# Performance work log

Measured on AMD Instinct MI355X. Metric: run time of the kernel, lower is better.

## Reference

```python
import jax, jax.numpy as jnp
import numpy as np
import math

D = 256          # cubic grid size
THICKNESS = 20   # sponge thickness
DT = 0.001
N_PML = 2
R_PML = 0.001


def _build_sigma(vmax, shape, thickness):
    # vectorized equivalent of the torch slab-assignment loop:
    # final value at a point is damping(min distance to any face) if < thickness else 0
    sigma0 = -(N_PML + 1) * vmax * math.log(R_PML) / (2.0 * thickness)
    dists = []
    for ax, n in enumerate(shape):
        idx = jnp.arange(n)
        d = jnp.minimum(idx, n - 1 - idx)
        sh = [1, 1, 1]
        sh[ax] = n
        dists.append(d.reshape(sh))
    mind = jnp.minimum(jnp.minimum(
        jnp.broadcast_to(dists[0], shape),
        jnp.broadcast_to(dists[1], shape)),
        jnp.broadcast_to(dists[2], shape)).astype(jnp.float32)
    damping = sigma0 * (1.0 - mind / thickness) ** N_PML
    return jnp.where(mind < thickness, damping, 0.0).astype(jnp.float32)


def setup_inputs() -> dict:
    key = jax.random.key(0)
    k1, k2, k3, k4 = jax.random.split(key, 4)
    shape = (D, D, D)
    source_cur = jax.random.normal(k1, shape, dtype=jnp.float32)
    p_cur = jax.random.normal(k2, shape, dtype=jnp.float32)
    p_pre = jax.random.normal(k3, shape, dtype=jnp.float32)
    v = 1500.0 + 1000.0 * jax.random.uniform(k4, shape, dtype=jnp.float32)
    a = v * v * (DT * DT)                      # v**2 * dt**2
    sigma = _build_sigma(float(jnp.max(v)), shape, THICKNESS)
    return {"source_cur": source_cur, "p_cur": p_cur, "p_pre": p_pre,
            "a": a, "sigma": sigma, "dt": DT}


def _laplacian7(p):
    # 7-point stencil with zero padding (matches conv3d(kernel, padding=1))
    pp = jnp.pad(p, 1)
    return (pp[2:, 1:-1, 1:-1] + pp[:-2, 1:-1, 1:-1]
            + pp[1:-1, 2:, 1:-1] + pp[1:-1, :-2, 1:-1]
            + pp[1:-1, 1:-1, 2:] + pp[1:-1, 1:-1, :-2]
            - 6.0 * p)


def reference(source_cur, p_cur, p_pre, a, sigma, dt):
    p_cur = p_cur + source_cur
    lap = _laplacian7(p_cur)
    half = 0.5 * sigma * dt
    p_new = (2.0 * p_cur - (1.0 - half) * p_pre + a * lap) / (1.0 + half)
    return (p_new, p_cur)
```

## Files before the change

### kernel.cpp

```cpp
#include <hip/hip_runtime.h>

#define DD 256
#define DD2 (DD * DD)
#define DD3 (DD * DD * DD)
#define TH 20
#define XSEG 8

typedef float f32x4 __attribute__((ext_vector_type(4)));

__device__ __forceinline__ f32x4 ld4_sum(const float* __restrict__ p,
                                         const float* __restrict__ s,
                                         int idx) {
    return *reinterpret_cast<const f32x4*>(p + idx) +
           *reinterpret_cast<const f32x4*>(s + idx);
}

__device__ __forceinline__ f32x4 rcp4(f32x4 x) {
    f32x4 r;
    r.x = __builtin_amdgcn_rcpf(x.x);
    r.y = __builtin_amdgcn_rcpf(x.y);
    r.z = __builtin_amdgcn_rcpf(x.z);
    r.w = __builtin_amdgcn_rcpf(x.w);
    return r;
}

__global__ __launch_bounds__(256) void sponge_kernel(
    const float* __restrict__ src,
    const float* __restrict__ pc,
    const float* __restrict__ pp,
    const float* __restrict__ aa,
    const float* __restrict__ sg,
    const float* __restrict__ dtp,
    float* __restrict__ out_pnew,
    float* __restrict__ out_pcur)
{
    const float dt = dtp[0];

    const int lane = threadIdx.x & 63;
    const int w    = threadIdx.x >> 6;

    const int wid   = (blockIdx.x & 7) * 64 + (blockIdx.x >> 3);
    const int ytile = wid & 15;
    const int xseg  = wid >> 4;
    const int y0    = ytile * 16 + w * 4;
    const int x0    = xseg * XSEG;
    const int basez = lane * 4;

    const bool zsp = (lane < TH / 4) | (lane >= (DD - TH + 3) / 4);

    f32x4 colA[6], colB[6], colC[6];

#pragma unroll
    for (int r = 0; r < 6; ++r) {
        const int yy = y0 - 1 + r;
        colA[r] = (f32x4)(0.0f);
        colB[r] = (f32x4)(0.0f);
        if (yy >= 0 && yy < DD) {
            if (x0 > 0) colA[r] = ld4_sum(pc, src, (x0 - 1) * DD2 + yy * DD + basez);
            colB[r] = ld4_sum(pc, src, x0 * DD2 + yy * DD + basez);
        }
    }

#pragma unroll
    for (int st = 0; st < XSEG; ++st) {
        const int x  = x0 + st;
        const int pb = x * DD2 + basez;

        f32x4 p4v[4], a4v[4];
#pragma unroll
        for (int r = 0; r < 4; ++r) {
            const int idx = pb + (y0 + r) * DD;
            p4v[r] = __builtin_nontemporal_load(reinterpret_cast<const f32x4*>(pp + idx));
            a4v[r] = __builtin_nontemporal_load(reinterpret_cast<const f32x4*>(aa + idx));
        }

        const bool xsp = (x < TH) | (x >= DD - TH);
        f32x4 s4v[4];
#pragma unroll
        for (int r = 0; r < 4; ++r) {
            const int yy = y0 + r;
            const bool sp = xsp | zsp | (yy < TH) | (yy >= DD - TH);
            s4v[r] = sp ? *reinterpret_cast<const f32x4*>(sg + pb + yy * DD)
                        : (f32x4)(0.0f);
        }

#pragma unroll
        for (int r = 0; r < 6; ++r) {
            const int yy = y0 - 1 + r;
            colC[r] = (f32x4)(0.0f);
            if (x < DD - 1 && yy >= 0 && yy < DD)
                colC[r] = ld4_sum(pc, src, (x + 1) * DD2 + yy * DD + basez);
        }

#pragma unroll
        for (int r = 0; r < 4; ++r) {
            const int idx = pb + (y0 + r) * DD;
            const f32x4 u = colB[r + 1];

            float left  = __shfl_up(u.w, 1);
            float right = __shfl_down(u.x, 1);
            if (lane == 0)  left  = 0.0f;
            if (lane == 63) right = 0.0f;

            f32x4 lap;
            lap.x = left  + u.y + colB[r].x + colB[r + 2].x + colA[r + 1].x + colC[r + 1].x - 6.0f * u.x;
            lap.y = u.x   + u.z + colB[r].y + colB[r + 2].y + colA[r + 1].y + colC[r + 1].y - 6.0f * u.y;
            lap.z = u.y   + u.w + colB[r].z + colB[r + 2].z + colA[r + 1].z + colC[r + 1].z - 6.0f * u.z;
            lap.w = u.z   + right + colB[r].w + colB[r + 2].w + colA[r + 1].w + colC[r + 1].w - 6.0f * u.w;

            const f32x4 half = (0.5f * dt) * s4v[r];
            const f32x4 num  = 2.0f * u - (1.0f - half) * p4v[r] + a4v[r] * lap;
            const f32x4 pn   = num * rcp4(1.0f + half);

            __builtin_nontemporal_store(pn, reinterpret_cast<f32x4*>(out_pnew + idx));
            __builtin_nontemporal_store(u,  reinterpret_cast<f32x4*>(out_pcur + idx));
        }

#pragma unroll
        for (int r = 0; r < 6; ++r) {
            colA[r] = colB[r];
            colB[r] = colC[r];
        }
    }
}

extern "C" void kernel_launch(void* const* d_in, const int* in_sizes, int n_in,
                              void* d_out, int out_size, void* d_ws, size_t ws_size,
                              hipStream_t stream) {
    const float* src = (const float*)d_in[0];
    const float* pc  = (const float*)d_in[1];
    const float* pp  = (const float*)d_in[2];
    const float* aa  = (const float*)d_in[3];
    const float* sg  = (const float*)d_in[4];
    const float* dtp = (const float*)d_in[5];
    float* out = (float*)d_out;

    const int grid = 16 * (DD / XSEG);
    sponge_kernel<<<grid, 256, 0, stream>>>(src, pc, pp, aa, sg, dtp,
                                            out, out + DD3);
}
```

Baseline: 85.73 us.

## Software-pipeline x-slab loads one step ahead and use single-wave blocks

Loads for the next x-plane (p_pre, a, sigma and the x+2 pressure column) are issued before computing the current plane, and the results are rotated through registers. This overlaps memory latency with the stencil arithmetic. Blocks are shrunk from four waves to one wave, and the grid is enlarged to keep the same per-thread tiling. The extra live vectors raise register pressure and may reduce occupancy.

```diff
diff --git a/kernel.cpp b/kernel.cpp
--- a/kernel.cpp
+++ b/kernel.cpp
@@ -24,7 +24,7 @@
     return r;
 }
 
-__global__ __launch_bounds__(256) void sponge_kernel(
+__global__ __launch_bounds__(64) void sponge_kernel(
     const float* __restrict__ src,
     const float* __restrict__ pc,
     const float* __restrict__ pp,
@@ -35,14 +35,12 @@
     float* __restrict__ out_pcur)
 {
     const float dt = dtp[0];
+    const int lane = threadIdx.x;
 
-    const int lane = threadIdx.x & 63;
-    const int w    = threadIdx.x >> 6;
-
-    const int wid   = (blockIdx.x & 7) * 64 + (blockIdx.x >> 3);
-    const int ytile = wid & 15;
-    const int xseg  = wid >> 4;
-    const int y0    = ytile * 16 + w * 4;
+    const int wid   = (blockIdx.x & 7) * 256 + (blockIdx.x >> 3);
+    const int ytile = wid & 63;
+    const int xseg  = wid >> 6;
+    const int y0    = ytile * 4;
     const int x0    = xseg * XSEG;
     const int basez = lane * 4;
 
@@ -55,9 +53,25 @@
         const int yy = y0 - 1 + r;
         colA[r] = (f32x4)(0.0f);
         colB[r] = (f32x4)(0.0f);
+        colC[r] = (f32x4)(0.0f);
         if (yy >= 0 && yy < DD) {
             if (x0 > 0) colA[r] = ld4_sum(pc, src, (x0 - 1) * DD2 + yy * DD + basez);
             colB[r] = ld4_sum(pc, src, x0 * DD2 + yy * DD + basez);
+            colC[r] = ld4_sum(pc, src, (x0 + 1) * DD2 + yy * DD + basez);
+        }
+    }
+
+    f32x4 pcur[4], acur[4], scur[4];
+    {
+        const int pb = x0 * DD2 + basez;
+        const bool xsp = (x0 < TH) | (x0 >= DD - TH);
+#pragma unroll
+        for (int r = 0; r < 4; ++r) {
+            const int idx = pb + (y0 + r) * DD;
+            pcur[r] = __builtin_nontemporal_load(reinterpret_cast<const f32x4*>(pp + idx));
+            acur[r] = __builtin_nontemporal_load(reinterpret_cast<const f32x4*>(aa + idx));
+            const bool sp = xsp | zsp | ((y0 + r) < TH) | ((y0 + r) >= DD - TH);
+            scur[r] = sp ? *reinterpret_cast<const f32x4*>(sg + idx) : (f32x4)(0.0f);
         }
     }
 
@@ -66,30 +80,26 @@
         const int x  = x0 + st;
         const int pb = x * DD2 + basez;
 
-        f32x4 p4v[4], a4v[4];
+        f32x4 colD[6], pnx[4], anx[4], snx[4];
+        if (st < XSEG - 1) {
+            const int xn  = x + 1;
+            const int pbn = xn * DD2 + basez;
+            const bool xspn = (xn < TH) | (xn >= DD - TH);
 #pragma unroll
-        for (int r = 0; r < 4; ++r) {
-            const int idx = pb + (y0 + r) * DD;
-            p4v[r] = __builtin_nontemporal_load(reinterpret_cast<const f32x4*>(pp + idx));
-            a4v[r] = __builtin_nontemporal_load(reinterpret_cast<const f32x4*>(aa + idx));
-        }
-
-        const bool xsp = (x < TH) | (x >= DD - TH);
-        f32x4 s4v[4];
+            for (int r = 0; r < 4; ++r) {
+                const int idx = pbn + (y0 + r) * DD;
+                pnx[r] = __builtin_nontemporal_load(reinterpret_cast<const f32x4*>(pp + idx));
+                anx[r] = __builtin_nontemporal_load(reinterpret_cast<const f32x4*>(aa + idx));
+                const bool sp = xspn | zsp | ((y0 + r) < TH) | ((y0 + r) >= DD - TH);
+                snx[r] = sp ? *reinterpret_cast<const f32x4*>(sg + idx) : (f32x4)(0.0f);
+            }
 #pragma unroll
-        for (int r = 0; r < 4; ++r) {
-            const int yy = y0 + r;
-            const bool sp = xsp | zsp | (yy < TH) | (yy >= DD - TH);
-            s4v[r] = sp ? *reinterpret_cast<const f32x4*>(sg + pb + yy * DD)
-                        : (f32x4)(0.0f);
-        }
-
-#pragma unroll
-        for (int r = 0; r < 6; ++r) {
-            const int yy = y0 - 1 + r;
-            colC[r] = (f32x4)(0.0f);
-            if (x < DD - 1 && yy >= 0 && yy < DD)
-                colC[r] = ld4_sum(pc, src, (x + 1) * DD2 + yy * DD + basez);
+            for (int r = 0; r < 6; ++r) {
+                const int yy = y0 - 1 + r;
+                colD[r] = (f32x4)(0.0f);
+                if ((x + 2) < DD && yy >= 0 && yy < DD)
+                    colD[r] = ld4_sum(pc, src, (x + 2) * DD2 + yy * DD + basez);
+            }
         }
 
 #pragma unroll
@@ -108,18 +118,27 @@
             lap.z = u.y   + u.w + colB[r].z + colB[r + 2].z + colA[r + 1].z + colC[r + 1].z - 6.0f * u.z;
             lap.w = u.z   + right + colB[r].w + colB[r + 2].w + colA[r + 1].w + colC[r + 1].w - 6.0f * u.w;
 
-            const f32x4 half = (0.5f * dt) * s4v[r];
-            const f32x4 num  = 2.0f * u - (1.0f - half) * p4v[r] + a4v[r] * lap;
+            const f32x4 half = (0.5f * dt) * scur[r];
+            const f32x4 num  = 2.0f * u - (1.0f - half) * pcur[r] + acur[r] * lap;
             const f32x4 pn   = num * rcp4(1.0f + half);
 
             __builtin_nontemporal_store(pn, reinterpret_cast<f32x4*>(out_pnew + idx));
             __builtin_nontemporal_store(u,  reinterpret_cast<f32x4*>(out_pcur + idx));
         }
 
+        if (st < XSEG - 1) {
 #pragma unroll
-        for (int r = 0; r < 6; ++r) {
-            colA[r] = colB[r];
-            colB[r] = colC[r];
+            for (int r = 0; r < 6; ++r) {
+                colA[r] = colB[r];
+                colB[r] = colC[r];
+                colC[r] = colD[r];
+            }
+#pragma unroll
+            for (int r = 0; r < 4; ++r) {
+                pcur[r] = pnx[r];
+                acur[r] = anx[r];
+                scur[r] = snx[r];
+            }
         }
     }
 }
@@ -135,7 +154,7 @@
     const float* dtp = (const float*)d_in[5];
     float* out = (float*)d_out;
 
-    const int grid = 16 * (DD / XSEG);
-    sponge_kernel<<<grid, 256, 0, stream>>>(src, pc, pp, aa, sg, dtp,
-                                            out, out + DD3);
+    const int grid = 64 * (DD / XSEG);
+    sponge_kernel<<<grid, 64, 0, stream>>>(src, pc, pp, aa, sg, dtp,
+                                           out, out + DD3);
 }
```

Result: no change. 86.05 us (+0.4%).
